# Kernel optimization log

Measured on AMD Instinct MI355X. Metric: run time of the kernel, lower is better.

Reference implementation:

```python
import jax, jax.numpy as jnp
import numpy as np

MAXDISP = 48  # maxdisp at feature resolution (192 full-res / 4)


def setup_inputs() -> dict:
    key = jax.random.key(0)
    k1, k2 = jax.random.split(key)
    B, C, H, W = 4, 32, 64, 128
    input_1 = jax.random.normal(k1, (B, C, H, W), dtype=jnp.float32)  # left/ref features
    input_2 = jax.random.normal(k2, (B, C, H, W), dtype=jnp.float32)  # right/target features
    return {"input_1": input_1, "input_2": input_2}


def _cost_volume(ref, tgt, maxdisp):
    # PSMNet-style concat cost volume:
    #   cost[:, :C, d, :, w] = ref[:, :, :, w]      for w >= d, else 0
    #   cost[:, C:, d, :, w] = tgt[:, :, :, w - d]  for w >= d, else 0
    B, C, H, W = ref.shape
    d = jnp.arange(maxdisp)[:, None]                 # [D, 1]
    w = jnp.arange(W)[None, :]                       # [1, W]
    mask = (w >= d).astype(ref.dtype)                # [D, W]
    idx = jnp.clip(w - d, 0, W - 1)                  # [D, W] gather indices into tgt width
    # ref plane: broadcast over D, zero where w < d
    ref_vol = ref[:, :, None, :, :] * mask[None, None, :, None, :]      # [B, C, D, H, W]
    # tgt plane: shift right by d via gather, zero where w < d
    tgt_vol = tgt[:, :, :, idx]                                          # [B, C, H, D, W]
    tgt_vol = jnp.moveaxis(tgt_vol, 3, 2) * mask[None, None, :, None, :]  # [B, C, D, H, W]
    return jnp.concatenate([ref_vol, tgt_vol], axis=1)                   # [B, 2C, D, H, W]


def reference(input_1, input_2):
    return _cost_volume(input_1, input_2, MAXDISP)
```

## Files before the change

### kernel.cpp

```cpp
#include <hip/hip_runtime.h>


constexpr int CV_B = 4;
constexpr int CV_C = 32;
constexpr int CV_H = 64;
constexpr int CV_W = 128;
constexpr int CV_D = 48;

typedef float floatx4 __attribute__((ext_vector_type(4)));

__global__ __launch_bounds__(256) void cost_volume_kernel(
    const float* __restrict__ ref,
    const float* __restrict__ tgt,
    floatx4* __restrict__ out)
{
    const int w4 = threadIdx.x & 31;
    const int d0 = threadIdx.x >> 5;
    const int h  = blockIdx.x & (CV_H - 1);
    const int bc = blockIdx.x >> 6;
    const int b  = bc >> 6;
    const int c2 = bc & 63;

    const bool is_tgt = (c2 >= CV_C);
    const int  c      = is_tgt ? (c2 - CV_C) : c2;

    const float* __restrict__ src =
        (is_tgt ? tgt : ref) + ((b * CV_C + c) * CV_H + h) * CV_W;

    const int w0 = w4 << 2;

    floatx4* __restrict__ o =
        out + (((bc * CV_D + d0) * CV_H + h) << 5) + w4;
    constexpr int OSTRIDE = 8 * CV_H * (CV_W / 4);

    if (!is_tgt) {
        const floatx4 v = *reinterpret_cast<const floatx4*>(src + w0);
#pragma unroll
        for (int k = 0; k < 6; ++k) {
            const int d = d0 + (k << 3);
            floatx4 r;
            r.x = (w0 + 0 >= d) ? v.x : 0.0f;
            r.y = (w0 + 1 >= d) ? v.y : 0.0f;
            r.z = (w0 + 2 >= d) ? v.z : 0.0f;
            r.w = (w0 + 3 >= d) ? v.w : 0.0f;
            __builtin_nontemporal_store(r, o + k * OSTRIDE);
        }
    } else {
#pragma unroll
        for (int k = 0; k < 6; ++k) {
            const int d = d0 + (k << 3);
            const int s = w0 - d;
            floatx4 r;
            if (s >= 0) {
                r = *reinterpret_cast<const floatx4*>(src + s);
            } else {
                floatx4 a;
#pragma unroll
                for (int j = 0; j < 4; ++j)
                    a[j] = (s + j >= 0) ? src[s + j] : 0.0f;
                r = a;
            }
            __builtin_nontemporal_store(r, o + k * OSTRIDE);
        }
    }
}

extern "C" void kernel_launch(void* const* d_in, const int* in_sizes, int n_in,
                              void* d_out, int out_size, void* d_ws, size_t ws_size,
                              hipStream_t stream)
{
    const float* ref = (const float*)d_in[0];
    const float* tgt = (const float*)d_in[1];
    floatx4* out = (floatx4*)d_out;

    dim3 block(256);
    dim3 grid(CV_B * 2 * CV_C * CV_H);
    cost_volume_kernel<<<grid, block, 0, stream>>>(ref, tgt, out);
}
```

Before: 69.62 us.

## Remap grid to one block per (disparity, batch-channel) plane with contiguous output writes

Reorganizes the work so each block handles one disparity slice of one (b, channel) pair across all 64 rows. The output plane it writes is contiguous, and the masks or shift are uniform per thread. Fully masked target lanes now store zeros without issuing loads. The aim is more coalesced, sequential write streams and cheaper per-element logic. The trade-off is that input rows are re-read once per disparity rather than reused from registers across six disparities. This relies on cache hits for those repeated reads.

After: 121.8 us. 75.0% more time.

```diff
diff --git a/kernel.cpp b/kernel.cpp
--- a/kernel.cpp
+++ b/kernel.cpp
@@ -14,53 +14,67 @@
     const float* __restrict__ tgt,
     floatx4* __restrict__ out)
 {
-    const int w4 = threadIdx.x & 31;
-    const int d0 = threadIdx.x >> 5;
-    const int h  = blockIdx.x & (CV_H - 1);
-    const int bc = blockIdx.x >> 6;
-    const int b  = bc >> 6;
-    const int c2 = bc & 63;
+    const int tid = threadIdx.x;
+    const int d   = blockIdx.x;
+    const int bc  = blockIdx.y;
+    const int b   = bc >> 6;
+    const int c2  = bc & 63;
 
     const bool is_tgt = (c2 >= CV_C);
     const int  c      = is_tgt ? (c2 - CV_C) : c2;
 
-    const float* __restrict__ src =
-        (is_tgt ? tgt : ref) + ((b * CV_C + c) * CV_H + h) * CV_W;
-
+    const int w4 = tid & 31;
+    const int hs = tid >> 5;
     const int w0 = w4 << 2;
 
-    floatx4* __restrict__ o =
-        out + (((bc * CV_D + d0) * CV_H + h) << 5) + w4;
-    constexpr int OSTRIDE = 8 * CV_H * (CV_W / 4);
+    const float* __restrict__ src =
+        (is_tgt ? tgt : ref) + (b * CV_C + c) * (CV_H * CV_W);
+
+    floatx4* __restrict__ o = out + (((bc * CV_D + d)) << 11) + tid;
 
     if (!is_tgt) {
-        const floatx4 v = *reinterpret_cast<const floatx4*>(src + w0);
+        const bool mx = (w0 + 0 >= d);
+        const bool my = (w0 + 1 >= d);
+        const bool mz = (w0 + 2 >= d);
+        const bool mw = (w0 + 3 >= d);
 #pragma unroll
-        for (int k = 0; k < 6; ++k) {
-            const int d = d0 + (k << 3);
+        for (int k = 0; k < 8; ++k) {
+            const int h = (k << 3) + hs;
+            const floatx4 v =
+                *reinterpret_cast<const floatx4*>(src + h * CV_W + w0);
             floatx4 r;
-            r.x = (w0 + 0 >= d) ? v.x : 0.0f;
-            r.y = (w0 + 1 >= d) ? v.y : 0.0f;
-            r.z = (w0 + 2 >= d) ? v.z : 0.0f;
-            r.w = (w0 + 3 >= d) ? v.w : 0.0f;
-            __builtin_nontemporal_store(r, o + k * OSTRIDE);
+            r.x = mx ? v.x : 0.0f;
+            r.y = my ? v.y : 0.0f;
+            r.z = mz ? v.z : 0.0f;
+            r.w = mw ? v.w : 0.0f;
+            __builtin_nontemporal_store(r, o + (k << 8));
         }
     } else {
+        const int s = w0 - d;
+        if (s >= 0) {
 #pragma unroll
-        for (int k = 0; k < 6; ++k) {
-            const int d = d0 + (k << 3);
-            const int s = w0 - d;
-            floatx4 r;
-            if (s >= 0) {
-                r = *reinterpret_cast<const floatx4*>(src + s);
-            } else {
-                floatx4 a;
+            for (int k = 0; k < 8; ++k) {
+                const int h = (k << 3) + hs;
+                const floatx4 v =
+                    *reinterpret_cast<const floatx4*>(src + h * CV_W + s);
+                __builtin_nontemporal_store(v, o + (k << 8));
+            }
+        } else if (s > -4) {
+#pragma unroll
+            for (int k = 0; k < 8; ++k) {
+                const int h = (k << 3) + hs;
+                const float* row = src + h * CV_W;
+                floatx4 r;
 #pragma unroll
                 for (int j = 0; j < 4; ++j)
-                    a[j] = (s + j >= 0) ? src[s + j] : 0.0f;
-                r = a;
+                    r[j] = (s + j >= 0) ? row[s + j] : 0.0f;
+                __builtin_nontemporal_store(r, o + (k << 8));
             }
-            __builtin_nontemporal_store(r, o + k * OSTRIDE);
+        } else {
+            const floatx4 z = {0.0f, 0.0f, 0.0f, 0.0f};
+#pragma unroll
+            for (int k = 0; k < 8; ++k)
+                __builtin_nontemporal_store(z, o + (k << 8));
         }
     }
 }
@@ -74,6 +88,6 @@
     floatx4* out = (floatx4*)d_out;
 
     dim3 block(256);
-    dim3 grid(CV_B * 2 * CV_C * CV_H);
+    dim3 grid(CV_D, CV_B * 2 * CV_C);
     cost_volume_kernel<<<grid, block, 0, stream>>>(ref, tgt, out);
 }
```
